# Performance work log

Hardware: AMD Instinct MI355X
Metric: run time of the kernel (lower is better)

The kernel has to match this reference:

```python
import jax, jax.numpy as jnp
import numpy as np

THR = 0.2          # config['thr']
BORDER_RM = 2      # config['border_rm']
TEMP = 0.1         # config['dsmax_temperature']


def setup_inputs() -> dict:
    key = jax.random.key(0)
    k0, k1 = jax.random.split(key)
    N, C = 2, 256
    h0c, w0c, h1c, w1c = 60, 80, 60, 80
    return {
        "feat_c0": jax.random.normal(k0, (N, h0c * w0c, C), dtype=jnp.float32),
        "feat_c1": jax.random.normal(k1, (N, h1c * w1c, C), dtype=jnp.float32),
        "h0c": h0c, "w0c": w0c, "h1c": h1c, "w1c": w1c,
    }


def _valid_1d(n: int, b: int):
    # True in the interior [b, n-b), False on the border — matches mask_border writes
    return jnp.zeros((n,), dtype=bool).at[b:n - b].set(True)


def reference(feat_c0, feat_c1, h0c, w0c, h1c, w1c):
    N, L, C = feat_c0.shape
    S = feat_c1.shape[1]
    scale = 1.0 / (C ** 0.5)
    f0 = feat_c0 * scale
    f1 = feat_c1 * scale

    # similarity + dual softmax  -> conf_matrix [N, L, S]
    sim = jnp.einsum('nlc,nsc->nls', f0, f1) / TEMP
    conf = jax.nn.softmax(sim, axis=1) * jax.nn.softmax(sim, axis=2)

    # threshold + border removal (mask_border, vectorized as an interior mask)
    mask = conf > THR
    b = BORDER_RM
    border = (_valid_1d(h0c, b)[:, None, None, None]
              & _valid_1d(w0c, b)[None, :, None, None]
              & _valid_1d(h1c, b)[None, None, :, None]
              & _valid_1d(w1c, b)[None, None, None, :])  # [h0c,w0c,h1c,w1c]
    mask = (mask.reshape(N, h0c, w0c, h1c, w1c) & border[None]).reshape(N, L, S)

    # mutual nearest neighbor
    mask = mask \
        & (conf == conf.max(axis=2, keepdims=True)) \
        & (conf == conf.max(axis=1, keepdims=True))

    # match extraction, expressed densely (static shapes for jit):
    # mask_v[b,i] = row i of pair b has a match; j_ids its column; mconf its confidence
    mask_v = mask.any(axis=2)                               # [N, L]
    j_ids = jnp.argmax(mask, axis=2)                        # [N, L] (first True)
    mconf = jnp.take_along_axis(conf, j_ids[:, :, None], axis=2)[..., 0]
    mconf = jnp.where(mask_v, mconf, 0.0)                   # [N, L]

    # coarse keypoint coords for matched columns: (x, y) = (j % w1c, j // w1c)
    mkpts1_c = jnp.stack([j_ids % w1c, j_ids // w1c], axis=-1)  # [N, L, 2]

    return conf, mask_v, j_ids, mkpts1_c, mconf
```

## Files before the change

kernel.cpp:

```cpp
#include <hip/hip_runtime.h>

typedef _Float16 half8 __attribute__((ext_vector_type(8)));
typedef float f32x4 __attribute__((ext_vector_type(4)));

#define NB 2
#define LS 4800
#define CCH 256
#define W0 80
#define W1 80
#define THRV 0.2f
#define SQS 0.19764235376052370f

#define TN 38
#define PADL 4864

#define OF_RST  0
#define OF_CST  19200
#define OF_RWM  38400
#define OF_CAND 48000
#define OF_CLM  57600
#define OF_PROW 67200
#define OF_PCOL (67200 + 739328)
#define OF_AH   (67200 + 2*739328)
#define OF_BH   (OF_AH + 1228800)

#define O_MASKV 46080000ull
#define O_JIDS  46089600ull
#define O_MKPT  46099200ull
#define O_MCONF 46118400ull

__device__ __forceinline__ void load_lds16(const void* g, void* l) {
    __builtin_amdgcn_global_load_lds((const __attribute__((address_space(1))) void*)g,
                                     (__attribute__((address_space(3))) void*)l, 16, 0, 0);
}

__global__ __launch_bounds__(256) void conv_half(const float* __restrict__ A,
                                                 const float* __restrict__ B,
                                                 float* __restrict__ ws) {
    const int which = blockIdx.y;
    const float* src = which ? B : A;
    _Float16* dst = (_Float16*)(ws + (which ? OF_BH : OF_AH));
    const int idx = blockIdx.x * 256 + threadIdx.x;
    const float4 v = ((const float4*)src)[idx];
    union { _Float16 h[4]; uint2 u; } p;
    p.h[0] = (_Float16)(v.x * SQS);
    p.h[1] = (_Float16)(v.y * SQS);
    p.h[2] = (_Float16)(v.z * SQS);
    p.h[3] = (_Float16)(v.w * SQS);
    ((uint2*)dst)[idx] = p.u;
}

__device__ __forceinline__ void gemm_core(const _Float16* __restrict__ Ah,
                                          const _Float16* __restrict__ Bh,
                                          _Float16* smA, _Float16* smB,
                                          const int bx, const int by,
                                          const int tid, f32x4 (&acc)[4][4]) {
    const int lane = tid & 63, w = tid >> 6;
    const int wx = w & 1, wy = w >> 1;
    const int m = lane & 15, quad = lane >> 4;
    const int srow = lane >> 3;
    const int qst = (lane & 7) ^ (srow & 7);

    for (int kt = 0; kt < 4; kt++) {
        const int k0 = kt * 64;
#pragma unroll
        for (int i = 0; i < 4; i++) {
            const int c = i * 4 + w;
            int gr = by * 128 + c * 8 + srow; gr = gr < LS ? gr : LS - 1;
            load_lds16(Ah + (size_t)gr * CCH + k0 + qst * 8, &smA[c * 512]);
        }
#pragma unroll
        for (int i = 0; i < 4; i++) {
            const int c = i * 4 + w;
            int gr = bx * 128 + c * 8 + srow; gr = gr < LS ? gr : LS - 1;
            load_lds16(Bh + (size_t)gr * CCH + k0 + qst * 8, &smB[c * 512]);
        }
        __syncthreads();
#pragma unroll
        for (int t = 0; t < 2; t++) {
            half8 Af[4], Bf[4];
#pragma unroll
            for (int a = 0; a < 4; a++) {
                const int rl = wy * 64 + a * 16 + m;
                const int sl = rl * 8 + ((t * 4 + quad) ^ (rl & 7));
                Af[a] = *(const half8*)&smA[sl * 8];
            }
#pragma unroll
            for (int b = 0; b < 4; b++) {
                const int cl = wx * 64 + b * 16 + m;
                const int sl = cl * 8 + ((t * 4 + quad) ^ (cl & 7));
                Bf[b] = *(const half8*)&smB[sl * 8];
            }
#pragma unroll
            for (int a = 0; a < 4; a++)
#pragma unroll
                for (int b = 0; b < 4; b++)
                    acc[a][b] = __builtin_amdgcn_mfma_f32_16x16x32_f16(Af[a], Bf[b], acc[a][b], 0, 0, 0);
        }
        __syncthreads();
    }
}

__global__ __launch_bounds__(256, 2) void gemm_stats(float* __restrict__ ws) {
    __shared__ __align__(16) union {
        struct { _Float16 A[8192]; _Float16 B[8192]; } st;
        struct { float rs[128][2][2]; float cs[128][2][2]; } red;
    } sm;
    const int bx = blockIdx.x, by = blockIdx.y, n = blockIdx.z;
    const _Float16* Ah = (const _Float16*)(ws + OF_AH) + (size_t)n * LS * CCH;
    const _Float16* Bh = (const _Float16*)(ws + OF_BH) + (size_t)n * LS * CCH;
    const int tid = threadIdx.x;
    const int lane = tid & 63, w = tid >> 6;
    const int wx = w & 1, wy = w >> 1;
    const int m = lane & 15, quad = lane >> 4;

    f32x4 acc[4][4];
    {
        f32x4 z = {0.f, 0.f, 0.f, 0.f};
#pragma unroll
        for (int a = 0; a < 4; a++)
#pragma unroll
            for (int b = 0; b < 4; b++) acc[a][b] = z;
    }
    gemm_core(Ah, Bh, sm.st.A, sm.st.B, bx, by, tid, acc);

    const int l0 = by * 128, s0 = bx * 128;
    bool bval[4];
#pragma unroll
    for (int b = 0; b < 4; b++) bval[b] = (s0 + wx * 64 + b * 16 + m) < LS;

    float T = -1e30f;
#pragma unroll
    for (int a = 0; a < 4; a++)
#pragma unroll
        for (int reg = 0; reg < 4; reg++) {
            if ((l0 + wy * 64 + a * 16 + quad * 4 + reg) < LS) {
#pragma unroll
                for (int b = 0; b < 4; b++)
                    if (bval[b]) T = fmaxf(T, acc[a][b][reg]);
            }
        }
#pragma unroll
    for (int d = 1; d < 64; d <<= 1) T = fmaxf(T, __shfl_xor(T, d, 64));

#pragma unroll
    for (int a = 0; a < 4; a++)
#pragma unroll
        for (int reg = 0; reg < 4; reg++) {
            const bool rv = (l0 + wy * 64 + a * 16 + quad * 4 + reg) < LS;
#pragma unroll
            for (int b = 0; b < 4; b++)
                acc[a][b][reg] = (rv && bval[b]) ? __expf(acc[a][b][reg] - T) : 0.f;
        }

#pragma unroll
    for (int a = 0; a < 4; a++)
#pragma unroll
        for (int reg = 0; reg < 4; reg++) {
            float s = acc[a][0][reg] + acc[a][1][reg] + acc[a][2][reg] + acc[a][3][reg];
#pragma unroll
            for (int d = 1; d < 16; d <<= 1) s += __shfl_xor(s, d, 64);
            if (m == 0) {
                const int rl = wy * 64 + a * 16 + quad * 4 + reg;
                sm.red.rs[rl][wx][0] = T; sm.red.rs[rl][wx][1] = s;
            }
        }
#pragma unroll
    for (int b = 0; b < 4; b++) {
        float s = 0.f;
#pragma unroll
        for (int a = 0; a < 4; a++)
#pragma unroll
            for (int reg = 0; reg < 4; reg++) s += acc[a][b][reg];
        s += __shfl_xor(s, 16, 64);
        s += __shfl_xor(s, 32, 64);
        if (quad == 0) {
            const int cl = wx * 64 + b * 16 + m;
            sm.red.cs[cl][wy][0] = T; sm.red.cs[cl][wy][1] = s;
        }
    }
    __syncthreads();
    if (tid < 128) {
        const float m0 = sm.red.rs[tid][0][0], v0 = sm.red.rs[tid][0][1];
        const float m1 = sm.red.rs[tid][1][0], v1 = sm.red.rs[tid][1][1];
        const float nm = fmaxf(m0, m1);
        const float s = v0 * __expf(m0 - nm) + v1 * __expf(m1 - nm);
        ((float2*)(ws + OF_PROW))[((size_t)n * TN + bx) * PADL + by * 128 + tid] = make_float2(nm, s);
    } else {
        const int t = tid - 128;
        const float m0 = sm.red.cs[t][0][0], v0 = sm.red.cs[t][0][1];
        const float m1 = sm.red.cs[t][1][0], v1 = sm.red.cs[t][1][1];
        const float nm = fmaxf(m0, m1);
        const float s = v0 * __expf(m0 - nm) + v1 * __expf(m1 - nm);
        ((float2*)(ws + OF_PCOL))[((size_t)n * TN + by) * PADL + bx * 128 + t] = make_float2(nm, s);
    }
}

__global__ __launch_bounds__(256) void combine_stats(float* __restrict__ ws) {
    const int idx = blockIdx.x * 256 + threadIdx.x;
    const int half_ = idx >= 9600;
    const int i = idx - half_ * 9600;
    const int n = i / LS, r = i % LS;
    const float2* P = (const float2*)(ws + (half_ ? OF_PCOL : OF_PROW)) + (size_t)n * TN * PADL + r;
    float M = -1e30f, S = 0.f;
    for (int b = 0; b < TN; b++) {
        const float2 p = P[(size_t)b * PADL];
        const float nm = fmaxf(M, p.x);
        S = S * __expf(M - nm) + p.y * __expf(p.x - nm);
        M = nm;
    }
    ((float2*)(ws + (half_ ? OF_CST : OF_RST)))[n * LS + r] = make_float2(M, 1.0f / S);
}

__global__ __launch_bounds__(256, 2) void gemm_conf(float* __restrict__ out,
                                                    float* __restrict__ ws) {
    __shared__ __align__(16) union {
        struct { _Float16 A[8192]; _Float16 B[8192]; } st;
        struct { float rst[128][2]; float cst[128][2];
                 float rsv[128][2][2]; float csv[128][2]; } ep;
    } sm;
    const int bx = blockIdx.x, by = blockIdx.y, n = blockIdx.z;
    const _Float16* Ah = (const _Float16*)(ws + OF_AH) + (size_t)n * LS * CCH;
    const _Float16* Bh = (const _Float16*)(ws + OF_BH) + (size_t)n * LS * CCH;
    const int tid = threadIdx.x;
    const int lane = tid & 63, w = tid >> 6;
    const int wx = w & 1, wy = w >> 1;
    const int m = lane & 15, quad = lane >> 4;

    f32x4 acc[4][4];
    {
        f32x4 z = {0.f, 0.f, 0.f, 0.f};
#pragma unroll
        for (int a = 0; a < 4; a++)
#pragma unroll
            for (int b = 0; b < 4; b++) acc[a][b] = z;
    }
    gemm_core(Ah, Bh, sm.st.A, sm.st.B, bx, by, tid, acc);

    const int l0 = by * 128, s0 = bx * 128;
    if (tid < 128) {
        int r = l0 + tid; r = r < LS ? r : LS - 1;
        const float2 v = ((const float2*)(ws + OF_RST))[n * LS + r];
        sm.ep.rst[tid][0] = v.x; sm.ep.rst[tid][1] = v.y;
    } else {
        const int t = tid - 128;
        int c = s0 + t; c = c < LS ? c : LS - 1;
        const float2 v = ((const float2*)(ws + OF_CST))[n * LS + c];
        sm.ep.cst[t][0] = v.x; sm.ep.cst[t][1] = v.y;
    }
    __syncthreads();

    float* On = out + (size_t)n * LS * LS;
    float colm[4] = {-1.f, -1.f, -1.f, -1.f};
    bool bval[4]; int gc4[4]; float cmx[4], csi[4];
#pragma unroll
    for (int b = 0; b < 4; b++) {
        const int cl = wx * 64 + b * 16 + m;
        gc4[b] = s0 + cl;
        bval[b] = gc4[b] < LS;
        cmx[b] = sm.ep.cst[cl][0]; csi[b] = sm.ep.cst[cl][1];
    }
#pragma unroll
    for (int a = 0; a < 4; a++) {
#pragma unroll
        for (int reg = 0; reg < 4; reg++) {
            const int rl = wy * 64 + a * 16 + quad * 4 + reg;
            const int gr = l0 + rl;
            const float rm = sm.ep.rst[rl][0], rsi = sm.ep.rst[rl][1];
            const bool rv = gr < LS;
            float bestv = -1.f; int besti = 0;
#pragma unroll
            for (int b = 0; b < 4; b++) {
                const float c = __expf(2.f * acc[a][b][reg] - rm - cmx[b]) * (rsi * csi[b]);
                if (rv && bval[b]) {
                    On[(size_t)gr * LS + gc4[b]] = c;
                    if (c > bestv) { bestv = c; besti = gc4[b]; }
                    colm[b] = fmaxf(colm[b], c);
                }
            }
#pragma unroll
            for (int d = 1; d < 16; d <<= 1) {
                const float ov = __shfl_xor(bestv, d, 64);
                const int oi = __shfl_xor(besti, d, 64);
                if (ov > bestv || (ov == bestv && oi < besti)) { bestv = ov; besti = oi; }
            }
            if (m == 0) {
                sm.ep.rsv[rl][wx][0] = bestv;
                sm.ep.rsv[rl][wx][1] = __int_as_float(besti);
            }
        }
    }
#pragma unroll
    for (int b = 0; b < 4; b++) {
        float v = colm[b];
        v = fmaxf(v, __shfl_xor(v, 16, 64));
        v = fmaxf(v, __shfl_xor(v, 32, 64));
        if (quad == 0) sm.ep.csv[wx * 64 + b * 16 + m][wy] = v;
    }
    __syncthreads();
    if (tid < 128) {
        const float v0 = sm.ep.rsv[tid][0][0]; const int i0 = __float_as_int(sm.ep.rsv[tid][0][1]);
        const float v1 = sm.ep.rsv[tid][1][0]; const int i1 = __float_as_int(sm.ep.rsv[tid][1][1]);
        float bv; int bi;
        if (v0 > v1 || (v0 == v1 && i0 <= i1)) { bv = v0; bi = i0; } else { bv = v1; bi = i1; }
        ((float2*)(ws + OF_PROW))[((size_t)n * TN + bx) * PADL + by * 128 + tid] =
            make_float2(bv, __int_as_float(bi));
    } else {
        const int t = tid - 128;
        const float v = fmaxf(sm.ep.csv[t][0], sm.ep.csv[t][1]);
        (ws + OF_PCOL)[((size_t)n * TN + by) * PADL + bx * 128 + t] = v;
    }
}

__global__ __launch_bounds__(256) void combine_max(float* __restrict__ ws) {
    const int idx = blockIdx.x * 256 + threadIdx.x;
    const int half_ = idx >= 9600;
    const int i = idx - half_ * 9600;
    const int n = i / LS, r = i % LS;
    if (!half_) {
        const float2* P = (const float2*)(ws + OF_PROW) + (size_t)n * TN * PADL + r;
        float bv = -2.f; int bi = 0;
        for (int b = 0; b < TN; b++) {
            const float2 p = P[(size_t)b * PADL];
            const int pi = __float_as_int(p.y);
            if (p.x > bv || (p.x == bv && pi < bi)) { bv = p.x; bi = pi; }
        }
        ws[OF_RWM + i] = bv;
        ((int*)ws)[OF_CAND + i] = bi;
    } else {
        const float* P = ws + OF_PCOL + (size_t)n * TN * PADL + r;
        float v = -2.f;
        for (int b = 0; b < TN; b++) v = fmaxf(v, P[(size_t)b * PADL]);
        ws[OF_CLM + i] = v;
    }
}

__global__ __launch_bounds__(256) void match_pass(const float* __restrict__ ws,
                                                  float* __restrict__ out) {
    const int idx = blockIdx.x * 256 + threadIdx.x;
    if (idx >= NB * LS) return;
    const int n = idx / LS, l = idx % LS;
    const float rwm = ws[OF_RWM + idx];
    const int cand = ((const int*)ws)[OF_CAND + idx];
    const float clm = ws[OF_CLM + n * LS + cand];
    const int y0 = l / W0, x0 = l % W0;
    const int y1 = cand / W1, x1 = cand % W1;
    const bool b0 = (y0 >= 2 && y0 < 58 && x0 >= 2 && x0 < 78);
    const bool b1 = (y1 >= 2 && y1 < 58 && x1 >= 2 && x1 < 78);
    const bool matched = (rwm > THRV) && b0 && b1 && (rwm == clm);
    const int j = matched ? cand : 0;
    out[O_MASKV + idx] = matched ? 1.f : 0.f;
    out[O_JIDS + idx] = (float)j;
    out[O_MKPT + (size_t)idx * 2 + 0] = (float)(j % W1);
    out[O_MKPT + (size_t)idx * 2 + 1] = (float)(j / W1);
    out[O_MCONF + idx] = matched ? rwm : 0.f;
}

extern "C" void kernel_launch(void* const* d_in, const int* in_sizes, int n_in,
                              void* d_out, int out_size, void* d_ws, size_t ws_size,
                              hipStream_t stream) {
    const float* f0 = (const float*)d_in[0];
    const float* f1 = (const float*)d_in[1];
    float* out = (float*)d_out;
    float* ws = (float*)d_ws;

    conv_half<<<dim3(2400, 2), 256, 0, stream>>>(f0, f1, ws);
    gemm_stats<<<dim3(TN, TN, NB), 256, 0, stream>>>(ws);
    combine_stats<<<75, 256, 0, stream>>>(ws);
    gemm_conf<<<dim3(TN, TN, NB), 256, 0, stream>>>(out, ws);
    combine_max<<<75, 256, 0, stream>>>(ws);
    match_pass<<<38, 256, 0, stream>>>(ws, out);
}
```

Measured before the change: 306.8 us.

## Swizzle GEMM workgroup order, transpose partial-stat layout, raise occupancy to 3

Remaps each workgroup's linear id so that consecutive ids are spread across the 8 XCDs in contiguous chunks, which is meant to improve L2 reuse of A/B tiles within each XCD. It also transposes the per-tile partial row/column stats so each combine thread reads its 38 partials contiguously rather than with a PADL stride. Launch bounds for both GEMM kernels go from 2 to 3 waves-per-EU minimum, which may force register spills. The combined changes trade possible spilling for better cache locality, though the transposed layout now makes the GEMM epilogue stores strided.

```diff
diff --git a/kernel.cpp b/kernel.cpp
--- a/kernel.cpp
+++ b/kernel.cpp
@@ -13,6 +13,8 @@
 
 #define TN 38
 #define PADL 4864
+#define NWG (TN * TN * NB)
+#define CPX (NWG / 8)
 
 #define OF_RST  0
 #define OF_CST  19200
@@ -32,6 +34,14 @@
 __device__ __forceinline__ void load_lds16(const void* g, void* l) {
     __builtin_amdgcn_global_load_lds((const __attribute__((address_space(1))) void*)g,
                                      (__attribute__((address_space(3))) void*)l, 16, 0, 0);
+}
+
+__device__ __forceinline__ void swizzle_ids(int& n, int& by, int& bx) {
+    const int orig = ((int)blockIdx.z * TN + (int)blockIdx.y) * TN + (int)blockIdx.x;
+    const int wg = (orig & 7) * CPX + (orig >> 3);
+    n = wg / (TN * TN);
+    const int rem = wg % (TN * TN);
+    by = rem / TN; bx = rem % TN;
 }
 
 __global__ __launch_bounds__(256) void conv_half(const float* __restrict__ A,
@@ -101,12 +111,13 @@
     }
 }
 
-__global__ __launch_bounds__(256, 2) void gemm_stats(float* __restrict__ ws) {
+__global__ __launch_bounds__(256, 3) void gemm_stats(float* __restrict__ ws) {
     __shared__ __align__(16) union {
         struct { _Float16 A[8192]; _Float16 B[8192]; } st;
         struct { float rs[128][2][2]; float cs[128][2][2]; } red;
     } sm;
-    const int bx = blockIdx.x, by = blockIdx.y, n = blockIdx.z;
+    int n, by, bx;
+    swizzle_ids(n, by, bx);
     const _Float16* Ah = (const _Float16*)(ws + OF_AH) + (size_t)n * LS * CCH;
     const _Float16* Bh = (const _Float16*)(ws + OF_BH) + (size_t)n * LS * CCH;
     const int tid = threadIdx.x;
@@ -185,14 +196,14 @@
         const float m1 = sm.red.rs[tid][1][0], v1 = sm.red.rs[tid][1][1];
         const float nm = fmaxf(m0, m1);
         const float s = v0 * __expf(m0 - nm) + v1 * __expf(m1 - nm);
-        ((float2*)(ws + OF_PROW))[((size_t)n * TN + bx) * PADL + by * 128 + tid] = make_float2(nm, s);
+        ((float2*)(ws + OF_PROW))[((size_t)n * PADL + by * 128 + tid) * TN + bx] = make_float2(nm, s);
     } else {
         const int t = tid - 128;
         const float m0 = sm.red.cs[t][0][0], v0 = sm.red.cs[t][0][1];
         const float m1 = sm.red.cs[t][1][0], v1 = sm.red.cs[t][1][1];
         const float nm = fmaxf(m0, m1);
         const float s = v0 * __expf(m0 - nm) + v1 * __expf(m1 - nm);
-        ((float2*)(ws + OF_PCOL))[((size_t)n * TN + by) * PADL + bx * 128 + t] = make_float2(nm, s);
+        ((float2*)(ws + OF_PCOL))[((size_t)n * PADL + bx * 128 + t) * TN + by] = make_float2(nm, s);
     }
 }
 
@@ -201,10 +212,10 @@
     const int half_ = idx >= 9600;
     const int i = idx - half_ * 9600;
     const int n = i / LS, r = i % LS;
-    const float2* P = (const float2*)(ws + (half_ ? OF_PCOL : OF_PROW)) + (size_t)n * TN * PADL + r;
+    const float2* P = (const float2*)(ws + (half_ ? OF_PCOL : OF_PROW)) + ((size_t)n * PADL + r) * TN;
     float M = -1e30f, S = 0.f;
     for (int b = 0; b < TN; b++) {
-        const float2 p = P[(size_t)b * PADL];
+        const float2 p = P[b];
         const float nm = fmaxf(M, p.x);
         S = S * __expf(M - nm) + p.y * __expf(p.x - nm);
         M = nm;
@@ -212,14 +223,15 @@
     ((float2*)(ws + (half_ ? OF_CST : OF_RST)))[n * LS + r] = make_float2(M, 1.0f / S);
 }
 
-__global__ __launch_bounds__(256, 2) void gemm_conf(float* __restrict__ out,
+__global__ __launch_bounds__(256, 3) void gemm_conf(float* __restrict__ out,
                                                     float* __restrict__ ws) {
     __shared__ __align__(16) union {
         struct { _Float16 A[8192]; _Float16 B[8192]; } st;
         struct { float rst[128][2]; float cst[128][2];
                  float rsv[128][2][2]; float csv[128][2]; } ep;
     } sm;
-    const int bx = blockIdx.x, by = blockIdx.y, n = blockIdx.z;
+    int n, by, bx;
+    swizzle_ids(n, by, bx);
     const _Float16* Ah = (const _Float16*)(ws + OF_AH) + (size_t)n * LS * CCH;
     const _Float16* Bh = (const _Float16*)(ws + OF_BH) + (size_t)n * LS * CCH;
     const int tid = threadIdx.x;
@@ -303,12 +315,12 @@
         const float v1 = sm.ep.rsv[tid][1][0]; const int i1 = __float_as_int(sm.ep.rsv[tid][1][1]);
         float bv; int bi;
         if (v0 > v1 || (v0 == v1 && i0 <= i1)) { bv = v0; bi = i0; } else { bv = v1; bi = i1; }
-        ((float2*)(ws + OF_PROW))[((size_t)n * TN + bx) * PADL + by * 128 + tid] =
+        ((float2*)(ws + OF_PROW))[((size_t)n * PADL + by * 128 + tid) * TN + bx] =
             make_float2(bv, __int_as_float(bi));
     } else {
         const int t = tid - 128;
         const float v = fmaxf(sm.ep.csv[t][0], sm.ep.csv[t][1]);
-        (ws + OF_PCOL)[((size_t)n * TN + by) * PADL + bx * 128 + t] = v;
+        (ws + OF_PCOL)[((size_t)n * PADL + bx * 128 + t) * TN + by] = v;
     }
 }
 
@@ -318,19 +330,19 @@
     const int i = idx - half_ * 9600;
     const int n = i / LS, r = i % LS;
     if (!half_) {
-        const float2* P = (const float2*)(ws + OF_PROW) + (size_t)n * TN * PADL + r;
+        const float2* P = (const float2*)(ws + OF_PROW) + ((size_t)n * PADL + r) * TN;
         float bv = -2.f; int bi = 0;
         for (int b = 0; b < TN; b++) {
-            const float2 p = P[(size_t)b * PADL];
+            const float2 p = P[b];
             const int pi = __float_as_int(p.y);
             if (p.x > bv || (p.x == bv && pi < bi)) { bv = p.x; bi = pi; }
         }
         ws[OF_RWM + i] = bv;
         ((int*)ws)[OF_CAND + i] = bi;
     } else {
-        const float* P = ws + OF_PCOL + (size_t)n * TN * PADL + r;
+        const float* P = ws + OF_PCOL + ((size_t)n * PADL + r) * TN;
         float v = -2.f;
-        for (int b = 0; b < TN; b++) v = fmaxf(v, P[(size_t)b * PADL]);
+        for (int b = 0; b < TN; b++) v = fmaxf(v, P[b]);
         ws[OF_CLM + i] = v;
     }
 }
```

Result: no change. 307.5 us (+0.2%).
